# Kernel tuning notes

Measured on AMD Instinct MI355X. Metric: run time of the kernel, lower is better.

Reference implementation:

```python
import jax, jax.numpy as jnp
import numpy as np

N = 100000
EPS = 1e-5

def gcn_conv(x, W, b, src, dst, n):
    # linear transform first (PyG GCNConv): [N, H]
    h = x @ W
    # add self-loops
    loop = jnp.arange(n, dtype=src.dtype)
    s = jnp.concatenate([src, loop])
    d = jnp.concatenate([dst, loop])
    # symmetric normalization deg^{-1/2}[s] * deg^{-1/2}[d]
    deg = jax.ops.segment_sum(jnp.ones_like(d, dtype=h.dtype), d, num_segments=n)
    dinv = jnp.where(deg > 0, jax.lax.rsqrt(jnp.maximum(deg, 1.0) * 0 + jnp.where(deg > 0, deg, 1.0)), 0.0)
    norm = dinv[s] * dinv[d]
    msg = h[s] * norm[:, None]          # gather + scale: [E+N, H]
    out = jax.ops.segment_sum(msg, d, num_segments=n)  # scatter-add
    return out + b

def batch_norm(x, gamma, beta):
    mu = jnp.mean(x, axis=0)
    var = jnp.mean((x - mu) ** 2, axis=0)  # biased var, as BatchNorm1d training
    return (x - mu) * jax.lax.rsqrt(var + EPS) * gamma + beta

def setup_inputs() -> dict:
    key = jax.random.key(0)
    ks = jax.random.split(key, 8)
    D, H, O = 64, 64, 32
    E = 1600000
    x = jax.random.normal(ks[0], (N, D), dtype=jnp.float32)
    edge_index = jax.random.randint(ks[1], (2, E), 0, N, dtype=jnp.int64)
    W1 = jax.random.normal(ks[2], (D, H), dtype=jnp.float32) / np.sqrt(D)
    b1 = jnp.zeros((H,), dtype=jnp.float32)
    W2 = jax.random.normal(ks[3], (H, H), dtype=jnp.float32) / np.sqrt(H)
    b2 = jnp.zeros((H,), dtype=jnp.float32)
    gamma1 = jnp.ones((H,), dtype=jnp.float32); beta1 = jnp.zeros((H,), dtype=jnp.float32)
    gamma2 = jnp.ones((H,), dtype=jnp.float32); beta2 = jnp.zeros((H,), dtype=jnp.float32)
    Wfc = jax.random.normal(ks[4], (H, O), dtype=jnp.float32) / np.sqrt(H)
    bfc = jnp.zeros((O,), dtype=jnp.float32)
    return {"x": x, "edge_index": edge_index, "W1": W1, "b1": b1, "gamma1": gamma1, "beta1": beta1,
            "W2": W2, "b2": b2, "gamma2": gamma2, "beta2": beta2, "Wfc": Wfc, "bfc": bfc}

def reference(x, edge_index, W1, b1, gamma1, beta1, W2, b2, gamma2, beta2, Wfc, bfc):
    src, dst = edge_index[0], edge_index[1]
    h = jax.nn.relu(gcn_conv(x, W1, b1, src, dst, N))
    h = batch_norm(h, gamma1, beta1)
    h = jax.nn.relu(gcn_conv(h, W2, b2, src, dst, N))
    h = batch_norm(h, gamma2, beta2)
    return h @ Wfc + bfc
```

## Files before the change

kernel.cpp:

```cpp
#include <hip/hip_runtime.h>
#include <hip/hip_bf16.h>
#include <cstdint>
#include <cstddef>

#define NBK 128
#define BKB 512

static __device__ __forceinline__ unsigned pack_bf16(float a, float b) {
  __hip_bfloat16 lo = __float2bfloat16(a), hi = __float2bfloat16(b);
  unsigned short ulo = *reinterpret_cast<unsigned short*>(&lo);
  unsigned short uhi = *reinterpret_cast<unsigned short*>(&hi);
  return ((unsigned)uhi << 16) | ulo;
}
static __device__ __forceinline__ float blo(unsigned u) {
  union { unsigned q; float f; } x; x.q = u << 16; return x.f;
}
static __device__ __forceinline__ float bhi(unsigned u) {
  union { unsigned q; float f; } x; x.q = u & 0xffff0000u; return x.f;
}


__launch_bounds__(256)
__global__ void bucket_kernel(const int* __restrict__ src, const int* __restrict__ dst,
                              int E, int cap, int nbk,
                              int* __restrict__ bcur, int* __restrict__ deg,
                              int* __restrict__ bkt_d, int* __restrict__ bkt_s) {
  __shared__ int cnt[NBK], base[NBK], gbase[NBK], curb[NBK], pbase[NBK];
  __shared__ int ptot_s;
  __shared__ int stg_d[3200], stg_s[3200];
  int t = threadIdx.x;
  int chunk = (E + BKB - 1) / BKB;
  int ebeg = blockIdx.x * chunk;
  int eend = min(E, ebeg + chunk);
  int nloc = eend - ebeg;
  for (int q = t; q < nbk; q += 256) { cnt[q] = 0; curb[q] = 0; }
  __syncthreads();

  int dl[13], sl[13];
  int nr = (nloc + 255) >> 8;
#pragma unroll 13
  for (int u = 0; u < nr; ++u) {
    int li = (u << 8) + t;
    bool v = li < nloc;
    int i = ebeg + (v ? li : 0);
    int d = v ? __builtin_nontemporal_load(&dst[i]) : 0;
    int s = v ? __builtin_nontemporal_load(&src[i]) : 0;
    dl[u] = d; sl[u] = s;
    if (v) {
      atomicAdd(&deg[d], 1);
      atomicAdd(&cnt[d >> 10], 1);
    }
  }
  __syncthreads();
  if (t == 0) {
    int run = 0, prun = 0;
    for (int q = 0; q < nbk; ++q) {
      base[q] = run;  run += cnt[q];
      pbase[q] = prun; prun += (cnt[q] + 15) & ~15;
    }
    ptot_s = prun;
  }
  __syncthreads();
  for (int q = t; q < nbk; q += 256) {
    int c = cnt[q];
    gbase[q] = (c > 0) ? atomicAdd(&bcur[q], (c + 15) & ~15) : 0;
  }
#pragma unroll 13
  for (int u = 0; u < nr; ++u) {
    int li = (u << 8) + t;
    if (li < nloc) {
      int b = dl[u] >> 10;
      int pos = atomicAdd(&curb[b], 1) + base[b];
      stg_d[pos] = dl[u]; stg_s[pos] = sl[u];
    }
  }
  __syncthreads();
  int ptot = ptot_s;
  for (int i = t; i < ptot; i += 256) {
    int lo = 0, hi = nbk - 1;
    while (lo < hi) {
      int mid = (lo + hi + 1) >> 1;
      if (pbase[mid] <= i) lo = mid; else hi = mid - 1;
    }
    int q = lo;
    int j = i - pbase[q];
    int dv = -1, sv = 0;
    if (j < cnt[q]) { dv = stg_d[base[q] + j]; sv = stg_s[base[q] + j]; }
    size_t o = (size_t)q * cap + gbase[q] + j;
    bkt_d[o] = dv;
    bkt_s[o] = sv;
  }
}

__global__ void scan1_kernel(const int* __restrict__ deg, int n, int* __restrict__ rowptr,
                             float* __restrict__ dinv, int* __restrict__ bsums) {
  __shared__ int sm[1024];
  int t = threadIdx.x;
  int gid = blockIdx.x * 1024 + t;
  int v = 0;
  if (gid < n) {
    v = deg[gid];
    dinv[gid] = rsqrtf((float)(v + 1));
  }
  sm[t] = v;
  __syncthreads();
  for (int off = 1; off < 1024; off <<= 1) {
    int x = (t >= off) ? sm[t - off] : 0;
    __syncthreads();
    sm[t] += x;
    __syncthreads();
  }
  if (gid < n) rowptr[gid] = sm[t] - v;
  if (t == 1023) bsums[blockIdx.x] = sm[1023];
}

__global__ void scan2_kernel(int* __restrict__ bsums, int nb) {
  __shared__ int sm[1024];
  int t = threadIdx.x;
  int v = (t < nb) ? bsums[t] : 0;
  sm[t] = v;
  __syncthreads();
  for (int off = 1; off < 1024; off <<= 1) {
    int x = (t >= off) ? sm[t - off] : 0;
    __syncthreads();
    sm[t] += x;
    __syncthreads();
  }
  if (t < nb) bsums[t] = sm[t] - v;
}

__global__ void scan3_kernel(int n, int E, int* __restrict__ rowptr,
                             const int* __restrict__ bsums) {
  int i = blockIdx.x * blockDim.x + threadIdx.x;
  if (i < n) rowptr[i] += bsums[i >> 10];
  if (i == 0) rowptr[n] = E;
}

__launch_bounds__(1024)
__global__ void scatter_l_kernel(const int* __restrict__ bkt_d, const int* __restrict__ bkt_s,
                                 const int* __restrict__ bcur, int cap, int n,
                                 const int* __restrict__ rowptr, int* __restrict__ adj) {
  __shared__ int cur[1024];
  int b = blockIdx.x;
  int nodebase = b << 10;
  int nn = min(1024, n - nodebase);
  int t = threadIdx.x;
  if (t < nn) cur[t] = rowptr[nodebase + t];
  __syncthreads();
  int cnt = bcur[b];
  const int* bd = bkt_d + (size_t)b * cap;
  const int* bs = bkt_s + (size_t)b * cap;
  for (int i = t; i < cnt; i += 1024) {
    int d = __builtin_nontemporal_load(&bd[i]);
    int s = __builtin_nontemporal_load(&bs[i]);
    if (d >= 0) {
      int pos = atomicAdd(&cur[d - nodebase], 1);
      adj[pos] = s;
    }
  }
}


template <int OUT, bool BF16OUT, bool BN, bool ABF16>
__launch_bounds__(256)
__global__ void gemm_kernel(const void* __restrict__ Ap, const float* __restrict__ W,
                            const float* __restrict__ bnacc,
                            const float* __restrict__ gamma, const float* __restrict__ beta,
                            const float* __restrict__ bias, const float* __restrict__ rowscale,
                            void* __restrict__ Cout, int n, float invn) {
  constexpr int OQ = OUT / 4;
  __shared__ float lds[64 * 65];
  __shared__ float sc_s[64], sh_s[64];
  int t = threadIdx.x;
  int row0 = blockIdx.x * 64;
  int rows = n - row0; if (rows > 64) rows = 64;

  if (BN) {
    if (t < 64) {
      float su = 0.f, sq = 0.f;
#pragma unroll
      for (int c = 0; c < 8; ++c) {
        su += bnacc[c * 128 + t];
        sq += bnacc[c * 128 + 64 + t];
      }
      float mu = su * invn;
      float var = sq * invn - mu * mu;
      float sc = gamma[t] * rsqrtf(var + 1e-5f);
      sc_s[t] = sc;
      sh_s[t] = fmaf(-mu, sc, beta[t]);
    }
    __syncthreads();
  }

  if (ABF16) {
    const uint4* A4 = (const uint4*)((const unsigned short*)Ap + (size_t)row0 * 64);
#pragma unroll
    for (int j = 0; j < 2; ++j) {
      int idx = t + j * 256;
      int r = idx >> 3, c8 = idx & 7;
      uint4 v = make_uint4(0, 0, 0, 0);
      if (r < rows) v = A4[idx];
      float f[8] = {blo(v.x), bhi(v.x), blo(v.y), bhi(v.y),
                    blo(v.z), bhi(v.z), blo(v.w), bhi(v.w)};
      float* p = &lds[r * 65 + c8 * 8];
#pragma unroll
      for (int q = 0; q < 8; ++q) {
        float xv = f[q];
        if (BN) xv = fmaf(xv, sc_s[c8 * 8 + q], sh_s[c8 * 8 + q]);
        p[q] = xv;
      }
    }
  } else {
    const float4* A4 = (const float4*)((const float*)Ap + (size_t)row0 * 64);
#pragma unroll
    for (int j = 0; j < 4; ++j) {
      int idx = t + j * 256;
      int r = idx >> 4, c4 = idx & 15;
      float4 v = make_float4(0.f, 0.f, 0.f, 0.f);
      if (r < rows) v = A4[idx];
      if (BN) {
        int c = c4 * 4;
        v.x = fmaf(v.x, sc_s[c + 0], sh_s[c + 0]);
        v.y = fmaf(v.y, sc_s[c + 1], sh_s[c + 1]);
        v.z = fmaf(v.z, sc_s[c + 2], sh_s[c + 2]);
        v.w = fmaf(v.w, sc_s[c + 3], sh_s[c + 3]);
      }
      float* p = &lds[r * 65 + c4 * 4];
      p[0] = v.x; p[1] = v.y; p[2] = v.z; p[3] = v.w;
    }
  }
  __syncthreads();

  const int w = __builtin_amdgcn_readfirstlane(t >> 6);
  const int r = t & 63;
  float acc[OQ];
#pragma unroll
  for (int o = 0; o < OQ; ++o) acc[o] = 0.f;
  const float* Ar = &lds[r * 65];
  const float* Wp = W + w * OQ;
  for (int k = 0; k < 64; ++k) {
    float a = Ar[k];
#pragma unroll
    for (int o = 0; o < OQ; ++o) acc[o] = fmaf(a, Wp[k * OUT + o], acc[o]);
  }
  if (rowscale) {
    int rr = row0 + r; if (rr >= n) rr = n - 1;
    float rs = rowscale[rr];
#pragma unroll
    for (int o = 0; o < OQ; ++o) acc[o] *= rs;
  }
  if (bias) {
    const float* Bp = bias + w * OQ;
#pragma unroll
    for (int o = 0; o < OQ; ++o) acc[o] += Bp[o];
  }

  if (r < rows) {
    if (BF16OUT) {
      unsigned pk[OQ / 2];
#pragma unroll
      for (int o2 = 0; o2 < OQ / 2; ++o2) pk[o2] = pack_bf16(acc[2 * o2], acc[2 * o2 + 1]);
      uint4* cp = (uint4*)((__hip_bfloat16*)Cout + (size_t)(row0 + r) * OUT + w * OQ);
#pragma unroll
      for (int j = 0; j < OQ / 8; ++j) {
        uint4 v; v.x = pk[j * 4]; v.y = pk[j * 4 + 1]; v.z = pk[j * 4 + 2]; v.w = pk[j * 4 + 3];
        cp[j] = v;
      }
    } else {
      float4* cp = (float4*)((float*)Cout + (size_t)(row0 + r) * OUT + w * OQ);
#pragma unroll
      for (int j = 0; j < OQ / 4; ++j)
        cp[j] = make_float4(acc[j * 4], acc[j * 4 + 1], acc[j * 4 + 2], acc[j * 4 + 3]);
    }
  }
}


__launch_bounds__(256, 8)
__global__ void agg_kernel(const __hip_bfloat16* __restrict__ g, const int* __restrict__ rowptr,
                           const int* __restrict__ adj, const float* __restrict__ dinv,
                           const float* __restrict__ bias, __hip_bfloat16* __restrict__ out,
                           float* __restrict__ bnacc, int n) {
  const int tid = threadIdx.x;
  const int lane = tid & 63;
  const int wave = tid >> 6;
  const int grp = lane >> 3;
  const int sub = lane & 7;
  const int gw = blockIdx.x * 4 + wave;

  const unsigned short* gu = (const unsigned short*)g;

  int d = gw * 8 + grp;
  int beg = rowptr[d];
  int k = rowptr[d + 1] - beg;
  float di = dinv[d];

  const uint4 v0 = *(const uint4*)(gu + (((size_t)d) << 6) + sub * 8);
  float acc[8];
  acc[0] = blo(v0.x); acc[1] = bhi(v0.x);
  acc[2] = blo(v0.y); acc[3] = bhi(v0.y);
  acc[4] = blo(v0.z); acc[5] = bhi(v0.z);
  acc[6] = blo(v0.w); acc[7] = bhi(v0.w);

  int kmax = k;
  kmax = max(kmax, __shfl_xor(kmax, 8));
  kmax = max(kmax, __shfl_xor(kmax, 16));
  kmax = max(kmax, __shfl_xor(kmax, 32));

  for (int j0 = 0; j0 < kmax; j0 += 8) {
    uint4 vv[8];
    float w[8];
#pragma unroll
    for (int u = 0; u < 8; ++u) {
      int idx = j0 + u;
      int aoff = (idx < k) ? idx : 0;
      int s = __builtin_nontemporal_load(&adj[beg + aoff]);
      unsigned su = ((unsigned)s < (unsigned)n) ? (unsigned)s : (unsigned)d;
      vv[u] = *(const uint4*)(gu + (((size_t)su) << 6) + sub * 8);
      w[u] = (idx < k) ? 1.f : 0.f;
    }
#pragma unroll
    for (int u = 0; u < 8; ++u) {
      acc[0] = fmaf(w[u], blo(vv[u].x), acc[0]);
      acc[1] = fmaf(w[u], bhi(vv[u].x), acc[1]);
      acc[2] = fmaf(w[u], blo(vv[u].y), acc[2]);
      acc[3] = fmaf(w[u], bhi(vv[u].y), acc[3]);
      acc[4] = fmaf(w[u], blo(vv[u].z), acc[4]);
      acc[5] = fmaf(w[u], bhi(vv[u].z), acc[5]);
      acc[6] = fmaf(w[u], blo(vv[u].w), acc[6]);
      acc[7] = fmaf(w[u], bhi(vv[u].w), acc[7]);
    }
  }

  float bias8[8];
  {
    const float4* bp = (const float4*)(bias + sub * 8);
    float4 b0 = bp[0], b1 = bp[1];
    bias8[0]=b0.x; bias8[1]=b0.y; bias8[2]=b0.z; bias8[3]=b0.w;
    bias8[4]=b1.x; bias8[5]=b1.y; bias8[6]=b1.z; bias8[7]=b1.w;
  }

  float o[8], s1[8], s2[8];
#pragma unroll
  for (int j = 0; j < 8; ++j) {
    float v = fmaf(acc[j], di, bias8[j]);
    v = fmaxf(v, 0.f);
    o[j] = v;
    s1[j] = v;
    s2[j] = v * v;
  }
  uint4 ov;
  ov.x = pack_bf16(o[0], o[1]); ov.y = pack_bf16(o[2], o[3]);
  ov.z = pack_bf16(o[4], o[5]); ov.w = pack_bf16(o[6], o[7]);
  *(uint4*)((unsigned short*)out + (((size_t)d) << 6) + sub * 8) = ov;

#pragma unroll
  for (int j = 0; j < 8; ++j) {
    s1[j] += __shfl_xor(s1[j], 8);  s2[j] += __shfl_xor(s2[j], 8);
    s1[j] += __shfl_xor(s1[j], 16); s2[j] += __shfl_xor(s2[j], 16);
    s1[j] += __shfl_xor(s1[j], 32); s2[j] += __shfl_xor(s2[j], 32);
  }
  __shared__ float redA[4][64], redB[4][64];
  if (lane < 8) {
#pragma unroll
    for (int j = 0; j < 8; ++j) {
      redA[wave][sub * 8 + j] = s1[j];
      redB[wave][sub * 8 + j] = s2[j];
    }
  }
  __syncthreads();
  if (tid < 64) {
    float a = redA[0][tid] + redA[1][tid] + redA[2][tid] + redA[3][tid];
    float b = redB[0][tid] + redB[1][tid] + redB[2][tid] + redB[3][tid];
    float* dst = bnacc + (blockIdx.x & 7) * 128;
    atomicAdd(&dst[tid], a);
    atomicAdd(&dst[64 + tid], b);
  }
}


extern "C" void kernel_launch(void* const* d_in, const int* in_sizes, int n_in,
                              void* d_out, int out_size, void* d_ws, size_t ws_size,
                              hipStream_t stream) {
  const float* x      = (const float*)d_in[0];
  const int*   ei     = (const int*)d_in[1];
  const float* W1     = (const float*)d_in[2];
  const float* b1     = (const float*)d_in[3];
  const float* gamma1 = (const float*)d_in[4];
  const float* beta1  = (const float*)d_in[5];
  const float* W2     = (const float*)d_in[6];
  const float* b2     = (const float*)d_in[7];
  const float* gamma2 = (const float*)d_in[8];
  const float* beta2  = (const float*)d_in[9];
  const float* Wfc    = (const float*)d_in[10];
  const float* bfc    = (const float*)d_in[11];

  int n = in_sizes[0] / 64;
  int E = in_sizes[1] / 2;
  const int* src = ei;
  const int* dst = ei + E;

  char* base = (char*)d_ws;
  size_t off = 0;
  auto alloc = [&](size_t bytes) -> char* {
    char* p = base + off;
    off += (bytes + 255) & ~(size_t)255;
    return p;
  };
  int*   rowptr = (int*)alloc((size_t)(n + 1) * 4);
  int*   adj    = (int*)alloc(((size_t)E + 64) * 4);
  int*   bsums  = (int*)alloc(1024 * 4);
  float* dinv   = (float*)alloc((size_t)n * 4);
  float* bn     = (float*)alloc(2048 * 4);
  int*   bcur   = (int*)alloc(NBK * 4);
  int*   deg    = (int*)alloc((size_t)n * 4);
  __hip_bfloat16* hbuf = (__hip_bfloat16*)alloc((size_t)n * 64 * 2);
  char*  rraw   = alloc((size_t)n * 64 * 4);
  __hip_bfloat16* rbuf = (__hip_bfloat16*)rraw;
  int nbk = (n + 1023) >> 10;
  int cap = 24576;
  int* bkt_d = (int*)rraw;
  int* bkt_s = bkt_d + (size_t)nbk * cap;
  (void)ws_size; (void)n_in; (void)out_size;

  hipMemsetAsync(bn, 0, 2048 * 4, stream);
  hipMemsetAsync(bcur, 0, NBK * 4, stream);
  hipMemsetAsync(deg, 0, (size_t)n * 4, stream);

  bucket_kernel<<<BKB, 256, 0, stream>>>(src, dst, E, cap, nbk, bcur, deg, bkt_d, bkt_s);
  int nb = (n + 1023) / 1024;
  scan1_kernel<<<nb, 1024, 0, stream>>>(deg, n, rowptr, dinv, bsums);
  scan2_kernel<<<1, 1024, 0, stream>>>(bsums, nb);
  scan3_kernel<<<(n + 255) / 256, 256, 0, stream>>>(n, E, rowptr, bsums);
  scatter_l_kernel<<<nbk, 1024, 0, stream>>>(bkt_d, bkt_s, bcur, cap, n, rowptr, adj);

  int gg = (n + 63) / 64;
  int ga = n / 32;
  float invn = 1.0f / (float)n;
  gemm_kernel<64, true, false, false><<<gg, 256, 0, stream>>>(
      x, W1, nullptr, nullptr, nullptr, nullptr, dinv, hbuf, n, 0.f);
  agg_kernel<<<ga, 256, 0, stream>>>(hbuf, rowptr, adj, dinv, b1, rbuf, bn, n);
  gemm_kernel<64, true, true, true><<<gg, 256, 0, stream>>>(
      rbuf, W2, bn, gamma1, beta1, nullptr, dinv, hbuf, n, invn);
  agg_kernel<<<ga, 256, 0, stream>>>(hbuf, rowptr, adj, dinv, b2, rbuf, bn + 1024, n);
  gemm_kernel<32, false, true, true><<<gg, 256, 0, stream>>>(
      rbuf, Wfc, bn + 1024, gamma2, beta2, bfc, nullptr, d_out, n, invn);
}
```

Before: 331.3 us.

## Compute per-node degrees and CSR offsets inside bucket scatter, drop global scans

The bucket kernel no longer does a global atomic degree increment per edge. It only accumulates per-bucket edge totals. A tiny single-block scan turns those totals into bucket bases, and the scatter kernel builds a shared-memory histogram of its bucket, scans it locally to produce rowptr and dinv, then places the adjacency entries. This removes 1.6M global atomics, the deg memset and three scan launches, at the cost of a second pass over each bucket's destination list in the scatter kernel.

After: 281.5 us. -15.0%, faster.

```diff
diff --git a/kernel.cpp b/kernel.cpp
--- a/kernel.cpp
+++ b/kernel.cpp
@@ -23,7 +23,7 @@
 __launch_bounds__(256)
 __global__ void bucket_kernel(const int* __restrict__ src, const int* __restrict__ dst,
                               int E, int cap, int nbk,
-                              int* __restrict__ bcur, int* __restrict__ deg,
+                              int* __restrict__ bcur, int* __restrict__ rcnt,
                               int* __restrict__ bkt_d, int* __restrict__ bkt_s) {
   __shared__ int cnt[NBK], base[NBK], gbase[NBK], curb[NBK], pbase[NBK];
   __shared__ int ptot_s;
@@ -46,10 +46,7 @@
     int d = v ? __builtin_nontemporal_load(&dst[i]) : 0;
     int s = v ? __builtin_nontemporal_load(&src[i]) : 0;
     dl[u] = d; sl[u] = s;
-    if (v) {
-      atomicAdd(&deg[d], 1);
-      atomicAdd(&cnt[d >> 10], 1);
-    }
+    if (v) atomicAdd(&cnt[d >> 10], 1);
   }
   __syncthreads();
   if (t == 0) {
@@ -63,7 +60,10 @@
   __syncthreads();
   for (int q = t; q < nbk; q += 256) {
     int c = cnt[q];
-    gbase[q] = (c > 0) ? atomicAdd(&bcur[q], (c + 15) & ~15) : 0;
+    if (c > 0) {
+      gbase[q] = atomicAdd(&bcur[q], (c + 15) & ~15);
+      atomicAdd(&rcnt[q], c);
+    } else gbase[q] = 0;
   }
 #pragma unroll 13
   for (int u = 0; u < nr; ++u) {
@@ -92,68 +92,72 @@
   }
 }
 
-__global__ void scan1_kernel(const int* __restrict__ deg, int n, int* __restrict__ rowptr,
-                             float* __restrict__ dinv, int* __restrict__ bsums) {
-  __shared__ int sm[1024];
+__global__ void bscan_kernel(const int* __restrict__ rcnt, int nbk, int* __restrict__ bbase,
+                             int E, int n, int* __restrict__ rowptr) {
+  __shared__ int sm[NBK];
   int t = threadIdx.x;
-  int gid = blockIdx.x * 1024 + t;
-  int v = 0;
-  if (gid < n) {
-    v = deg[gid];
-    dinv[gid] = rsqrtf((float)(v + 1));
-  }
+  int v = (t < nbk) ? rcnt[t] : 0;
   sm[t] = v;
   __syncthreads();
-  for (int off = 1; off < 1024; off <<= 1) {
+  for (int off = 1; off < NBK; off <<= 1) {
     int x = (t >= off) ? sm[t - off] : 0;
     __syncthreads();
     sm[t] += x;
     __syncthreads();
   }
-  if (gid < n) rowptr[gid] = sm[t] - v;
-  if (t == 1023) bsums[blockIdx.x] = sm[1023];
-}
-
-__global__ void scan2_kernel(int* __restrict__ bsums, int nb) {
-  __shared__ int sm[1024];
-  int t = threadIdx.x;
-  int v = (t < nb) ? bsums[t] : 0;
-  sm[t] = v;
-  __syncthreads();
-  for (int off = 1; off < 1024; off <<= 1) {
-    int x = (t >= off) ? sm[t - off] : 0;
-    __syncthreads();
-    sm[t] += x;
-    __syncthreads();
-  }
-  if (t < nb) bsums[t] = sm[t] - v;
-}
-
-__global__ void scan3_kernel(int n, int E, int* __restrict__ rowptr,
-                             const int* __restrict__ bsums) {
-  int i = blockIdx.x * blockDim.x + threadIdx.x;
-  if (i < n) rowptr[i] += bsums[i >> 10];
-  if (i == 0) rowptr[n] = E;
+  if (t < nbk) bbase[t] = sm[t] - v;
+  if (t == 0) rowptr[n] = E;
 }
 
 __launch_bounds__(1024)
-__global__ void scatter_l_kernel(const int* __restrict__ bkt_d, const int* __restrict__ bkt_s,
-                                 const int* __restrict__ bcur, int cap, int n,
-                                 const int* __restrict__ rowptr, int* __restrict__ adj) {
+__global__ void scatter2_kernel(const int* __restrict__ bkt_d, const int* __restrict__ bkt_s,
+                                const int* __restrict__ bcur, const int* __restrict__ bbase,
+                                int cap, int n,
+                                int* __restrict__ rowptr, float* __restrict__ dinv,
+                                int* __restrict__ adj) {
+  __shared__ int hist[1024];
   __shared__ int cur[1024];
   int b = blockIdx.x;
   int nodebase = b << 10;
   int nn = min(1024, n - nodebase);
   int t = threadIdx.x;
-  if (t < nn) cur[t] = rowptr[nodebase + t];
-  __syncthreads();
+  hist[t] = 0;
+  __syncthreads();
+
   int cnt = bcur[b];
   const int* bd = bkt_d + (size_t)b * cap;
   const int* bs = bkt_s + (size_t)b * cap;
+
   for (int i = t; i < cnt; i += 1024) {
-    int d = __builtin_nontemporal_load(&bd[i]);
-    int s = __builtin_nontemporal_load(&bs[i]);
+    int d = bd[i];
+    if (d >= 0) atomicAdd(&hist[d - nodebase], 1);
+  }
+  __syncthreads();
+
+  int deg = hist[t];
+  int v = deg;
+  cur[t] = v;
+  __syncthreads();
+  for (int off = 1; off < 1024; off <<= 1) {
+    int x = (t >= off) ? cur[t - off] : 0;
+    __syncthreads();
+    cur[t] += x;
+    __syncthreads();
+  }
+  int excl = cur[t] - v;
+  int gb = bbase[b];
+  if (t < nn) {
+    rowptr[nodebase + t] = gb + excl;
+    dinv[nodebase + t] = rsqrtf((float)(deg + 1));
+  }
+  __syncthreads();
+  cur[t] = gb + excl;
+  __syncthreads();
+
+  for (int i = t; i < cnt; i += 1024) {
+    int d = bd[i];
     if (d >= 0) {
+      int s = bs[i];
       int pos = atomicAdd(&cur[d - nodebase], 1);
       adj[pos] = s;
     }
@@ -409,11 +413,11 @@
   };
   int*   rowptr = (int*)alloc((size_t)(n + 1) * 4);
   int*   adj    = (int*)alloc(((size_t)E + 64) * 4);
-  int*   bsums  = (int*)alloc(1024 * 4);
   float* dinv   = (float*)alloc((size_t)n * 4);
   float* bn     = (float*)alloc(2048 * 4);
   int*   bcur   = (int*)alloc(NBK * 4);
-  int*   deg    = (int*)alloc((size_t)n * 4);
+  int*   rcnt   = (int*)alloc(NBK * 4);
+  int*   bbase  = (int*)alloc(NBK * 4);
   __hip_bfloat16* hbuf = (__hip_bfloat16*)alloc((size_t)n * 64 * 2);
   char*  rraw   = alloc((size_t)n * 64 * 4);
   __hip_bfloat16* rbuf = (__hip_bfloat16*)rraw;
@@ -425,14 +429,12 @@
 
   hipMemsetAsync(bn, 0, 2048 * 4, stream);
   hipMemsetAsync(bcur, 0, NBK * 4, stream);
-  hipMemsetAsync(deg, 0, (size_t)n * 4, stream);
-
-  bucket_kernel<<<BKB, 256, 0, stream>>>(src, dst, E, cap, nbk, bcur, deg, bkt_d, bkt_s);
-  int nb = (n + 1023) / 1024;
-  scan1_kernel<<<nb, 1024, 0, stream>>>(deg, n, rowptr, dinv, bsums);
-  scan2_kernel<<<1, 1024, 0, stream>>>(bsums, nb);
-  scan3_kernel<<<(n + 255) / 256, 256, 0, stream>>>(n, E, rowptr, bsums);
-  scatter_l_kernel<<<nbk, 1024, 0, stream>>>(bkt_d, bkt_s, bcur, cap, n, rowptr, adj);
+  hipMemsetAsync(rcnt, 0, NBK * 4, stream);
+
+  bucket_kernel<<<BKB, 256, 0, stream>>>(src, dst, E, cap, nbk, bcur, rcnt, bkt_d, bkt_s);
+  bscan_kernel<<<1, NBK, 0, stream>>>(rcnt, nbk, bbase, E, n, rowptr);
+  scatter2_kernel<<<nbk, 1024, 0, stream>>>(bkt_d, bkt_s, bcur, bbase, cap, n,
+                                            rowptr, dinv, adj);
 
   int gg = (n + 63) / 64;
   int ga = n / 32;
```
